# Kernel tuning notes

Hardware: AMD Instinct MI355X
Metric: run time of the kernel (lower is better)

The kernel has to match this reference:

```python
import jax, jax.numpy as jnp
import numpy as np
from jax import lax

# --- COSMO-SAC constants (defaults from the layer) ---
T = 623.15
Q0 = 79.53
R0 = 66.69
C_HB = 85580.0
RGAS = 8.3144598 / 4184.0
SIG_HB = 0.0084
EPS = 3.667
AEFF = 7.5
EO = 0.0002395
ZC = 10.0
X0 = 0.235
X1 = 1.0 - 0.235
N_SIGMA = 51
N_ITERS = 50


def _deltaw():
    s = np.linspace(-0.025, 0.025, N_SIGMA)
    sigma_m = np.tile(s, (N_SIGMA, 1))          # rows of grid values
    sigma_n = sigma_m.T
    sigma_acc = np.tril(sigma_n) + np.triu(sigma_m, 1)
    sigma_don = np.tril(sigma_m) + np.triu(sigma_n, 1)
    fpol = (EPS - 1.0) / (EPS + 0.5)
    alpha = 0.3 * AEFF ** 1.5 / EO
    alpha_prime = fpol * alpha
    dw = (alpha_prime / 2.0 * (sigma_m + sigma_n) ** 2
          + C_HB * np.maximum(0.0, sigma_acc - SIG_HB) * np.minimum(0.0, sigma_don + SIG_HB))
    return jnp.asarray(dw, jnp.float32)

DELTAW = _deltaw()                       # [51,51]
SSS = jnp.exp(-DELTAW / (RGAS * T))      # [51,51]


def get_Gamma(psigma):
    """50-step fixed-point solve. psigma: [B,51] -> Gamma: [B,51]."""
    AA = SSS[None, :, :] * psigma[:, None, :]   # [B,51,51]
    def step(G, _):
        Gnew = 1.0 / jnp.einsum('bmn,bn->bm', AA, G)
        return (Gnew + G) * 0.5, None
    G, _ = lax.scan(step, jnp.ones_like(psigma), None, length=N_ITERS)
    return G


def setup_inputs() -> dict:
    key = jax.random.key(0)
    k1, k2, k3, k4 = jax.random.split(key, 4)
    B = 32768
    return {
        "input_my_sigma": jax.random.uniform(k1, (B, N_SIGMA), dtype=jnp.float32),
        "v_compound": jax.random.uniform(k2, (B,), dtype=jnp.float32),
        "input_vt_sigma": jax.random.uniform(k3, (B, N_SIGMA, 2), dtype=jnp.float32),
        "v_vt": jax.random.uniform(k4, (B,), dtype=jnp.float32),
    }


def reference(input_my_sigma, v_compound, input_vt_sigma, v_vt):
    my = input_my_sigma                 # [B,51]
    vt = input_vt_sigma[:, :, 1]        # [B,51]
    A0 = jnp.sum(my, axis=1)            # [B]
    A1 = jnp.sum(vt, axis=1)            # [B]

    psigma_mix = (X0 * my + X1 * vt) / (X0 * A0[:, None] + X1 * A1[:, None])
    lnGamma_mix = jnp.log(get_Gamma(psigma_mix))       # [B,51]

    # residual part for component i = 0
    psigma = my / A0[:, None]
    lnGammai = jnp.log(get_Gamma(psigma))              # [B,51]
    lng_resid = A0 / AEFF * jnp.sum(psigma * (lnGamma_mix - lnGammai), axis=1)

    # combinatorial part (Staverman-Guggenheim)
    q0 = A0 / Q0
    q1 = A1 / Q0
    r0 = v_compound / R0
    r1 = v_vt / R0
    xq = X0 * q0 + X1 * q1
    xr = X0 * r0 + X1 * r1
    theta = X0 * q0 / xq
    phi = X0 * r0 / xr
    l0 = ZC / 2.0 * (r0 - q0) - (r0 - 1.0)
    l1 = ZC / 2.0 * (r1 - q1) - (r1 - 1.0)
    xl = X0 * l0 + X1 * l1
    lng_comb = (jnp.log(phi / X0) + ZC / 2.0 * q0 * jnp.log(theta / phi)
                + l0 - phi / X0 * xl)

    return (lng_resid + lng_comb)[:, None]             # [B,1]
```

## Files before the change

kernel.cpp:

```cpp
#include <hip/hip_runtime.h>

typedef __bf16 bf16;
typedef __attribute__((ext_vector_type(4))) bf16 bf16x4;
typedef __attribute__((ext_vector_type(8))) bf16 bf16x8;
typedef __attribute__((ext_vector_type(4))) float f32x4;

namespace {

constexpr double csqrt(double x) {
  double s = x > 1 ? x : 1;
  for (int i = 0; i < 60; ++i) s = 0.5 * (s + x / s);
  return s;
}
constexpr double AP_D =
    ((3.667 - 1.0) / (3.667 + 0.5)) * (0.3 * (7.5 * csqrt(7.5)) / 0.0002395);
constexpr double RGAST_D = (8.3144598 / 4184.0) * 623.15;

__device__ __forceinline__ float sss_val(int i, int j) {
  if (i > 50 || j > 50) return 0.0f;
  const float si = -0.025f + 0.001f * (float)i;
  const float sj = -0.025f + 0.001f * (float)j;
  const float acc = fmaxf(0.0f, fmaxf(si, sj) - 0.0084f);
  const float don = fminf(0.0f, fminf(si, sj) + 0.0084f);
  const float dw = (float)(AP_D * 0.5) * (si + sj) * (si + sj) + 85580.0f * acc * don;
  return expf(-dw * (float)(1.0 / RGAST_D));
}

__device__ __forceinline__ float fast_log(float x) {
  return __builtin_amdgcn_logf(x) * 0.69314718056f;
}

__device__ __forceinline__ f32x4 mfma16(bf16x8 a, bf16x8 b, f32x4 c) {
  return __builtin_amdgcn_mfma_f32_16x16x32_bf16(a, b, c, 0, 0, 0);
}

}

__global__ __launch_bounds__(256, 4) void cosmo_mfma16(
    const float* __restrict__ my_sigma,
    const float* __restrict__ v_comp,
    const float* __restrict__ vt_sigma,
    const float* __restrict__ v_vt,
    float* __restrict__ out,
    int B)
{
  __shared__ bf16 lds[4][16 * 72];

  const int lane = threadIdx.x & 63;
  const int wv   = threadIdx.x >> 6;
  const int s    = lane & 15;
  const int g    = lane >> 4;
  const int e    = blockIdx.x * 32 + wv * 8 + (s >> 1);
  const int task = s & 1;
  const bool ein = (e < B);
  const int  ec  = ein ? e : 0;

  float myv[16], vtv[16];
#pragma unroll
  for (int t = 0; t < 4; ++t)
#pragma unroll
    for (int r = 0; r < 4; ++r) {
      const int n  = 16 * t + 4 * g + r;
      const bool nv = (n < 51) && ein;
      const int nc = (n < 51) ? n : 50;
      myv[4 * t + r] = nv ? my_sigma[(size_t)ec * 51 + nc] : 0.0f;
      vtv[4 * t + r] = nv ? vt_sigma[((size_t)ec * 51 + nc) * 2 + 1] : 0.0f;
    }

  float pA0 = 0.f, pA1 = 0.f;
#pragma unroll
  for (int i = 0; i < 16; ++i) { pA0 += myv[i]; pA1 += vtv[i]; }
  float A0 = pA0; A0 += __shfl_xor(A0, 16, 64); A0 += __shfl_xor(A0, 32, 64);
  float A1 = pA1; A1 += __shfl_xor(A1, 16, 64); A1 += __shfl_xor(A1, 32, 64);

  const float den  = task ? (0.235f * A0 + 0.765f * A1) : A0;
  const float rden = __builtin_amdgcn_rcpf(den);
  const float rA0  = __builtin_amdgcn_rcpf(A0);

  float wC[16], G[16];
#pragma unroll
  for (int i = 0; i < 16; ++i) {
    const float num = task ? (0.235f * myv[i] + 0.765f * vtv[i]) : myv[i];
    wC[i] = num * rden;
    G[i]  = 1.0f;
  }

  bf16x8 afr[4][2];
#pragma unroll
  for (int t = 0; t < 4; ++t)
#pragma unroll
    for (int kt = 0; kt < 2; ++kt) {
      bf16x8 v;
#pragma unroll
      for (int i = 0; i < 8; ++i)
        v[i] = (bf16)sss_val(16 * t + s, 32 * kt + 8 * g + i);
      afr[t][kt] = v;
    }

  bf16* slab = &lds[wv][0];
  const int wb = s * 72 + 4 * g;
  const int rb = s * 72 + 8 * g;
  const float gpad = (g == 0) ? 0.0f : 1.0f;

#pragma unroll 1
  for (int it = 0; it < 50; ++it) {
#pragma unroll
    for (int t = 0; t < 4; ++t) {
      bf16x4 hv;
#pragma unroll
      for (int r = 0; r < 4; ++r)
        hv[r] = (bf16)(wC[4 * t + r] * G[4 * t + r]);
      *(bf16x4*)(slab + wb + 16 * t) = hv;
    }

    const bf16x8 bfr0 = *(const bf16x8*)(slab + rb);
    const bf16x8 bfr1 = *(const bf16x8*)(slab + rb + 32);

    const f32x4 z = {};
    f32x4 acc[4];
#pragma unroll
    for (int t = 0; t < 4; ++t) acc[t] = mfma16(afr[t][0], bfr0, z);
#pragma unroll
    for (int t = 0; t < 4; ++t) acc[t] = mfma16(afr[t][1], bfr1, acc[t]);

#pragma unroll
    for (int t = 0; t < 3; ++t)
#pragma unroll
      for (int r = 0; r < 4; ++r)
        G[4 * t + r] = 0.5f * (G[4 * t + r] + __builtin_amdgcn_rcpf(acc[t][r]));
#pragma unroll
    for (int r = 0; r < 4; ++r) {
      const float d = acc[3][r] + ((r < 3) ? gpad : 1.0f);
      G[12 + r] = 0.5f * (G[12 + r] + __builtin_amdgcn_rcpf(d));
    }
  }

  float Sp = 0.f;
#pragma unroll
  for (int t = 0; t < 4; ++t)
#pragma unroll
    for (int r = 0; r < 4; ++r) {
      const int n = 16 * t + 4 * g + r;
      if (n < 51) {
        const float p = (ein ? my_sigma[(size_t)ec * 51 + n] : 0.0f) * rA0;
        Sp += p * __builtin_amdgcn_logf(G[4 * t + r]);
      }
    }
  Sp += __shfl_xor(Sp, 16, 64);
  Sp += __shfl_xor(Sp, 32, 64);
  const float St = Sp * 0.69314718056f;
  const float So = __shfl_xor(St, 1, 64);

  if (task == 0 && g == 0 && ein) {
    const float lng_resid = A0 * (1.0f / 7.5f) * (So - St);
    const float v0  = v_comp[e];
    const float v1v = v_vt[e];
    const float q0 = A0 * (1.0f / 79.53f), q1 = A1 * (1.0f / 79.53f);
    const float r0 = v0 * (1.0f / 66.69f), r1 = v1v * (1.0f / 66.69f);
    const float xq = 0.235f * q0 + 0.765f * q1;
    const float xr = 0.235f * r0 + 0.765f * r1;
    const float theta = 0.235f * q0 * __builtin_amdgcn_rcpf(xq);
    const float phi   = 0.235f * r0 * __builtin_amdgcn_rcpf(xr);
    const float l0 = 5.0f * (r0 - q0) - (r0 - 1.0f);
    const float l1 = 5.0f * (r1 - q1) - (r1 - 1.0f);
    const float xl = 0.235f * l0 + 0.765f * l1;
    const float lng_comb = fast_log(phi * (1.0f / 0.235f))
                         + 5.0f * q0 * fast_log(theta * __builtin_amdgcn_rcpf(phi))
                         + l0 - (phi * (1.0f / 0.235f)) * xl;
    out[e] = lng_resid + lng_comb;
  }
}

extern "C" void kernel_launch(void* const* d_in, const int* in_sizes, int n_in,
                              void* d_out, int out_size, void* d_ws, size_t ws_size,
                              hipStream_t stream) {
  const float* my  = (const float*)d_in[0];
  const float* vc  = (const float*)d_in[1];
  const float* vts = (const float*)d_in[2];
  const float* vvt = (const float*)d_in[3];
  float* out = (float*)d_out;
  const int B = in_sizes[1];
  const int grid = (B + 31) / 32;
  cosmo_mfma16<<<grid, 256, 0, stream>>>(my, vc, vts, vvt, out, B);
}
```

Measured before the change: 127.5 us.

## Track wC-scaled Gamma in fixed-point loop and use single-wave blocks

The iteration now carries Gt = wC*G, so each step writes Gt straight to LDS and updates it with one fma on the reciprocal. This removes the per-element multiply before the bf16 store inside the 50-step loop. The true Gamma is recovered once at the end by dividing by wC, which is risky if an input weight is zero. Blocks shrink from four waves to one, and the LDS row stride drops from 72 to 68 with reads split into two 4-element loads, which changes scheduling granularity and bank mapping.

```diff
diff --git a/kernel.cpp b/kernel.cpp
--- a/kernel.cpp
+++ b/kernel.cpp
@@ -36,7 +36,7 @@
 
 }
 
-__global__ __launch_bounds__(256, 4) void cosmo_mfma16(
+__global__ __launch_bounds__(64, 4) void cosmo_mfma_gt(
     const float* __restrict__ my_sigma,
     const float* __restrict__ v_comp,
     const float* __restrict__ vt_sigma,
@@ -44,46 +44,47 @@
     float* __restrict__ out,
     int B)
 {
-  __shared__ bf16 lds[4][16 * 72];
+  __shared__ bf16 lds[16 * 68];
 
-  const int lane = threadIdx.x & 63;
-  const int wv   = threadIdx.x >> 6;
+  const int lane = threadIdx.x;
   const int s    = lane & 15;
   const int g    = lane >> 4;
-  const int e    = blockIdx.x * 32 + wv * 8 + (s >> 1);
+  const int e    = blockIdx.x * 8 + (s >> 1);
   const int task = s & 1;
   const bool ein = (e < B);
   const int  ec  = ein ? e : 0;
 
-  float myv[16], vtv[16];
+  float A0, A1, wC[16];
+  {
+    float myv[16], vtv[16];
 #pragma unroll
-  for (int t = 0; t < 4; ++t)
+    for (int t = 0; t < 4; ++t)
 #pragma unroll
-    for (int r = 0; r < 4; ++r) {
-      const int n  = 16 * t + 4 * g + r;
-      const bool nv = (n < 51) && ein;
-      const int nc = (n < 51) ? n : 50;
-      myv[4 * t + r] = nv ? my_sigma[(size_t)ec * 51 + nc] : 0.0f;
-      vtv[4 * t + r] = nv ? vt_sigma[((size_t)ec * 51 + nc) * 2 + 1] : 0.0f;
+      for (int r = 0; r < 4; ++r) {
+        const int n  = 16 * t + 4 * g + r;
+        const bool nv = (n < 51) && ein;
+        const int nc = (n < 51) ? n : 50;
+        myv[4 * t + r] = nv ? my_sigma[(size_t)ec * 51 + nc] : 0.0f;
+        vtv[4 * t + r] = nv ? vt_sigma[((size_t)ec * 51 + nc) * 2 + 1] : 0.0f;
+      }
+    float pA0 = 0.f, pA1 = 0.f;
+#pragma unroll
+    for (int i = 0; i < 16; ++i) { pA0 += myv[i]; pA1 += vtv[i]; }
+    A0 = pA0; A0 += __shfl_xor(A0, 16, 64); A0 += __shfl_xor(A0, 32, 64);
+    A1 = pA1; A1 += __shfl_xor(A1, 16, 64); A1 += __shfl_xor(A1, 32, 64);
+
+    const float den  = task ? (0.235f * A0 + 0.765f * A1) : A0;
+    const float rden = __builtin_amdgcn_rcpf(den);
+#pragma unroll
+    for (int i = 0; i < 16; ++i) {
+      const float num = task ? (0.235f * myv[i] + 0.765f * vtv[i]) : myv[i];
+      wC[i] = num * rden;
     }
+  }
 
-  float pA0 = 0.f, pA1 = 0.f;
+  float Gt[16];
 #pragma unroll
-  for (int i = 0; i < 16; ++i) { pA0 += myv[i]; pA1 += vtv[i]; }
-  float A0 = pA0; A0 += __shfl_xor(A0, 16, 64); A0 += __shfl_xor(A0, 32, 64);
-  float A1 = pA1; A1 += __shfl_xor(A1, 16, 64); A1 += __shfl_xor(A1, 32, 64);
-
-  const float den  = task ? (0.235f * A0 + 0.765f * A1) : A0;
-  const float rden = __builtin_amdgcn_rcpf(den);
-  const float rA0  = __builtin_amdgcn_rcpf(A0);
-
-  float wC[16], G[16];
-#pragma unroll
-  for (int i = 0; i < 16; ++i) {
-    const float num = task ? (0.235f * myv[i] + 0.765f * vtv[i]) : myv[i];
-    wC[i] = num * rden;
-    G[i]  = 1.0f;
-  }
+  for (int i = 0; i < 16; ++i) Gt[i] = wC[i];
 
   bf16x8 afr[4][2];
 #pragma unroll
@@ -97,10 +98,11 @@
       afr[t][kt] = v;
     }
 
-  bf16* slab = &lds[wv][0];
-  const int wb = s * 72 + 4 * g;
-  const int rb = s * 72 + 8 * g;
-  const float gpad = (g == 0) ? 0.0f : 1.0f;
+  const int wb = s * 68 + 4 * g;
+  const int rb = s * 68 + 8 * g;
+  float padd[4];
+#pragma unroll
+  for (int r = 0; r < 4; ++r) padd[r] = (4 * g + r >= 3) ? 1.0f : 0.0f;
 
 #pragma unroll 1
   for (int it = 0; it < 50; ++it) {
@@ -108,33 +110,42 @@
     for (int t = 0; t < 4; ++t) {
       bf16x4 hv;
 #pragma unroll
-      for (int r = 0; r < 4; ++r)
-        hv[r] = (bf16)(wC[4 * t + r] * G[4 * t + r]);
-      *(bf16x4*)(slab + wb + 16 * t) = hv;
+      for (int r = 0; r < 4; ++r) hv[r] = (bf16)Gt[4 * t + r];
+      *(bf16x4*)(lds + wb + 16 * t) = hv;
     }
 
-    const bf16x8 bfr0 = *(const bf16x8*)(slab + rb);
-    const bf16x8 bfr1 = *(const bf16x8*)(slab + rb + 32);
+    bf16x8 bfr[2];
+#pragma unroll
+    for (int kt = 0; kt < 2; ++kt) {
+      const bf16x4 lo = *(const bf16x4*)(lds + rb + 32 * kt);
+      const bf16x4 hi = *(const bf16x4*)(lds + rb + 32 * kt + 4);
+      bfr[kt] = __builtin_shufflevector(lo, hi, 0, 1, 2, 3, 4, 5, 6, 7);
+    }
 
     const f32x4 z = {};
     f32x4 acc[4];
 #pragma unroll
-    for (int t = 0; t < 4; ++t) acc[t] = mfma16(afr[t][0], bfr0, z);
+    for (int t = 0; t < 4; ++t) acc[t] = mfma16(afr[t][0], bfr[0], z);
 #pragma unroll
-    for (int t = 0; t < 4; ++t) acc[t] = mfma16(afr[t][1], bfr1, acc[t]);
+    for (int t = 0; t < 4; ++t) acc[t] = mfma16(afr[t][1], bfr[1], acc[t]);
 
 #pragma unroll
     for (int t = 0; t < 3; ++t)
 #pragma unroll
-      for (int r = 0; r < 4; ++r)
-        G[4 * t + r] = 0.5f * (G[4 * t + r] + __builtin_amdgcn_rcpf(acc[t][r]));
+      for (int r = 0; r < 4; ++r) {
+        const int i = 4 * t + r;
+        const float rc = __builtin_amdgcn_rcpf(acc[t][r]);
+        Gt[i] = 0.5f * __builtin_fmaf(wC[i], rc, Gt[i]);
+      }
 #pragma unroll
     for (int r = 0; r < 4; ++r) {
-      const float d = acc[3][r] + ((r < 3) ? gpad : 1.0f);
-      G[12 + r] = 0.5f * (G[12 + r] + __builtin_amdgcn_rcpf(d));
+      const int i = 12 + r;
+      const float rc = __builtin_amdgcn_rcpf(acc[3][r] + padd[r]);
+      Gt[i] = 0.5f * __builtin_fmaf(wC[i], rc, Gt[i]);
     }
   }
 
+  const float rA0 = __builtin_amdgcn_rcpf(A0);
   float Sp = 0.f;
 #pragma unroll
   for (int t = 0; t < 4; ++t)
@@ -142,8 +153,10 @@
     for (int r = 0; r < 4; ++r) {
       const int n = 16 * t + 4 * g + r;
       if (n < 51) {
-        const float p = (ein ? my_sigma[(size_t)ec * 51 + n] : 0.0f) * rA0;
-        Sp += p * __builtin_amdgcn_logf(G[4 * t + r]);
+        const int i = 4 * t + r;
+        const float p  = (ein ? my_sigma[(size_t)ec * 51 + n] : 0.0f) * rA0;
+        const float gg = Gt[i] * __builtin_amdgcn_rcpf(wC[i]);
+        Sp += p * __builtin_amdgcn_logf(gg);
       }
     }
   Sp += __shfl_xor(Sp, 16, 64);
@@ -180,6 +193,6 @@
   const float* vvt = (const float*)d_in[3];
   float* out = (float*)d_out;
   const int B = in_sizes[1];
-  const int grid = (B + 31) / 32;
-  cosmo_mfma16<<<grid, 256, 0, stream>>>(my, vc, vts, vvt, out, B);
+  const int grid = (B + 7) / 8;
+  cosmo_mfma_gt<<<grid, 64, 0, stream>>>(my, vc, vts, vvt, out, B);
 }
```

After: 122.6 us. -3.8%, faster.
